# Optimization experiments

Hardware: AMD Instinct MI355X
Metric: run time of the kernel (lower is better)

The kernel has to match this reference:

```python
import jax, jax.numpy as jnp
import numpy as np

N_LAYER = 4
N_HEAD = 16
N_EMBD = 1024
BLOCK = 1024
VOCAB = 100
TRANS = 16          # obs_dim + action_dim + 2 = 11 + 3 + 2
OBS_DIM = 11
ACT_DIM = 3
B, T = 2, 1024
VTOT = VOCAB * TRANS + 1  # token embedding rows
LN_EPS = 1e-5


def _layernorm(x, w, b):
    mu = jnp.mean(x, axis=-1, keepdims=True)
    var = jnp.var(x, axis=-1, keepdims=True)
    return (x - mu) * jax.lax.rsqrt(var + LN_EPS) * w + b


def _build_mask(t):
    # causal tril with every (joined_dim-1 mod joined_dim) column zeroed
    jd = OBS_DIM + ACT_DIM + 2  # 16
    m = jnp.tril(jnp.ones((t, t), dtype=bool))
    cols = jnp.arange(t)
    m = m & ((cols % jd) != (jd - 1))[None, :]
    return m  # [T, T] bool, True = keep


def setup_inputs() -> dict:
    key = jax.random.key(0)
    ks = jax.random.split(key, 24)
    C, L, F4 = N_EMBD, N_LAYER, 4 * N_EMBD
    g = lambda k, s: jax.random.normal(k, s, dtype=jnp.float32) * 0.02
    return {
        "tokens": jax.random.randint(ks[0], (B, T), 0, VTOT),
        "tok_emb": g(ks[1], (VTOT, C)),
        "pos_emb": g(ks[2], (1, BLOCK, C)),
        "Wq": g(ks[3], (L, C, C)), "bq": jnp.zeros((L, C), jnp.float32),
        "Wk": g(ks[4], (L, C, C)), "bk": jnp.zeros((L, C), jnp.float32),
        "Wv": g(ks[5], (L, C, C)), "bv": jnp.zeros((L, C), jnp.float32),
        "Wp": g(ks[6], (L, C, C)), "bp": jnp.zeros((L, C), jnp.float32),
        "ln1w": jnp.ones((L, C), jnp.float32), "ln1b": jnp.zeros((L, C), jnp.float32),
        "ln2w": jnp.ones((L, C), jnp.float32), "ln2b": jnp.zeros((L, C), jnp.float32),
        "W1": g(ks[7], (L, C, F4)), "b1": jnp.zeros((L, F4), jnp.float32),
        "W2": g(ks[8], (L, F4, C)), "b2": jnp.zeros((L, C), jnp.float32),
        "lnfw": jnp.ones((C,), jnp.float32), "lnfb": jnp.zeros((C,), jnp.float32),
        "head_w": g(ks[9], (TRANS, VOCAB + 1, C)),
    }


def _forward(tokens, tok_emb, pos_emb, Wq, bq, Wk, bk, Wv, bv, Wp, bp,
             ln1w, ln1b, ln2w, ln2b, W1, b1, W2, b2, lnfw, lnfb, head_w):
    b, t = tokens.shape
    C, H = N_EMBD, N_HEAD
    D = C // H
    scale = 1.0 / np.sqrt(D)
    mask = _build_mask(t)[None, None]  # [1,1,T,T]

    x = tok_emb[tokens] + pos_emb[:, :t, :]  # [B,T,C]
    for i in range(N_LAYER):
        h = _layernorm(x, ln1w[i], ln1b[i])
        q = (h @ Wq[i] + bq[i]).reshape(b, t, H, D).transpose(0, 2, 1, 3)
        k = (h @ Wk[i] + bk[i]).reshape(b, t, H, D).transpose(0, 2, 1, 3)
        v = (h @ Wv[i] + bv[i]).reshape(b, t, H, D).transpose(0, 2, 1, 3)
        att = jnp.einsum('bhtd,bhsd->bhts', q, k) * scale  # attn_bias=None => +0
        att = jnp.where(mask, att, -jnp.inf)
        att = jax.nn.softmax(att, axis=-1)
        y = jnp.einsum('bhts,bhsd->bhtd', att, v)
        y = y.transpose(0, 2, 1, 3).reshape(b, t, C)
        x = x + (y @ Wp[i] + bp[i])
        h2 = _layernorm(x, ln2w[i], ln2b[i])
        x = x + (jax.nn.gelu(h2 @ W1[i] + b1[i], approximate=False) @ W2[i] + b2[i])

    x = _layernorm(x, lnfw, lnfb)
    # pad_to_full_observation + EinLinear head
    n_pad = (TRANS - t % TRANS) % TRANS
    if n_pad:
        x = jnp.concatenate([x, jnp.zeros((b, n_pad, C), x.dtype)], axis=1)
    x_pad = x.reshape(-1, TRANS, C)                    # [b*n_states, TRANS, C]
    logits = jnp.einsum('eoi,bei->beo', head_w, x_pad)  # EinLinear, bias=False
    logits = logits.reshape(b, t + n_pad, VOCAB + 1)[:, :t]
    return logits


def reference(tokens, tok_emb, pos_emb, Wq, bq, Wk, bk, Wv, bv, Wp, bp,
              ln1w, ln1b, ln2w, ln2b, W1, b1, W2, b2, lnfw, lnfb, head_w):
    return _forward(tokens, tok_emb, pos_emb, Wq, bq, Wk, bk, Wv, bv, Wp, bp,
                    ln1w, ln1b, ln2w, ln2b, W1, b1, W2, b2, lnfw, lnfb, head_w)
```

## Files before the change

### kernel.cpp

```cpp
#include <hip/hip_runtime.h>
#include <hip/hip_bf16.h>
#include <math.h>

typedef unsigned short u16;
typedef __attribute__((ext_vector_type(8))) short short8;
typedef __attribute__((ext_vector_type(4))) short short4v;
typedef __attribute__((ext_vector_type(4))) float f32x4;

#define CDIM 1024
#define TDIM 1024
#define NROWS 2048
#define HEADS 16
#define HD 64
#define F4 4096

__device__ __forceinline__ u16 f2bf(float f) {
    union { float f; unsigned u; } v; v.f = f;
    unsigned r = v.u + 0x7fffu + ((v.u >> 16) & 1u);
    return (u16)(r >> 16);
}
__device__ __forceinline__ float bf2f(u16 h) {
    union { unsigned u; float f; } v; v.u = (unsigned)h << 16; return v.f;
}

__device__ __forceinline__ void gload_lds16(const void* g, void* lds) {
    __builtin_amdgcn_global_load_lds(
        (const __attribute__((address_space(1))) unsigned int*)g,
        (__attribute__((address_space(3))) unsigned int*)lds,
        16, 0, 0);
}

__device__ __forceinline__ void tile_map(int& bx, int& by, int& bz)
{
    const int gx = gridDim.x, gy = gridDim.y;
    const int fid = blockIdx.x + gx * (blockIdx.y + gy * blockIdx.z);
    const int nwg = gx * gy * gridDim.z;
    const int q = nwg >> 3, r = nwg & 7;
    const int xcd = fid & 7, t = fid >> 3;
    const int n = ((xcd < r) ? xcd * (q + 1) : r * (q + 1) + (xcd - r) * q) + t;
    const int nxy = gx * gy;
    bz = n / nxy;
    const int xy = n - bz * nxy;
    const int per_group = gx << 3;
    const int grp = xy / per_group;
    const int in = xy - grp * per_group;
    const int y0 = grp << 3;
    const int rem = gy - y0;
    const int gh = rem < 8 ? rem : 8;
    by = y0 + (in % gh);
    bx = in / gh;
}

__global__ __launch_bounds__(256)
void embed_k(const int* __restrict__ tok, const float* __restrict__ te,
             const float* __restrict__ pe, float* __restrict__ X)
{
    const int row = blockIdx.x;
    const int t = row & (TDIM - 1);
    const int tk = tok[row];
    const int c = threadIdx.x * 4;
    float4 a = *reinterpret_cast<const float4*>(te + (size_t)tk * CDIM + c);
    float4 b = *reinterpret_cast<const float4*>(pe + (size_t)t * CDIM + c);
    a.x += b.x; a.y += b.y; a.z += b.z; a.w += b.w;
    *reinterpret_cast<float4*>(X + (size_t)row * CDIM + c) = a;
}

template<bool BF16OUT>
__global__ __launch_bounds__(256)
void ln_k(const float* __restrict__ X, const float* __restrict__ g,
          const float* __restrict__ be, void* __restrict__ outp)
{
    __shared__ float red[4], red2[4];
    const int row = blockIdx.x, tid = threadIdx.x;
    const float* xr = X + (size_t)row * CDIM;
    const int c = tid * 4;
    float4 xv = *reinterpret_cast<const float4*>(xr + c);
    float s  = xv.x + xv.y + xv.z + xv.w;
    float s2 = xv.x*xv.x + xv.y*xv.y + xv.z*xv.z + xv.w*xv.w;
    #pragma unroll
    for (int off = 32; off; off >>= 1) {
        s  += __shfl_xor(s, off);
        s2 += __shfl_xor(s2, off);
    }
    if ((tid & 63) == 0) { red[tid >> 6] = s; red2[tid >> 6] = s2; }
    __syncthreads();
    const float ts  = red[0] + red[1] + red[2] + red[3];
    const float ts2 = red2[0] + red2[1] + red2[2] + red2[3];
    const float mu  = ts * (1.0f / CDIM);
    const float var = ts2 * (1.0f / CDIM) - mu * mu;
    const float rs  = rsqrtf(var + 1e-5f);
    float4 gv = *reinterpret_cast<const float4*>(g + c);
    float4 bv = *reinterpret_cast<const float4*>(be + c);
    float o0 = (xv.x - mu) * rs * gv.x + bv.x;
    float o1 = (xv.y - mu) * rs * gv.y + bv.y;
    float o2 = (xv.z - mu) * rs * gv.z + bv.z;
    float o3 = (xv.w - mu) * rs * gv.w + bv.w;
    if (BF16OUT) {
        u16 tmp[4] = { f2bf(o0), f2bf(o1), f2bf(o2), f2bf(o3) };
        u16* o = (u16*)outp + (size_t)row * CDIM + c;
        *reinterpret_cast<uint2*>(o) = *reinterpret_cast<const uint2*>(tmp);
    } else {
        float4 ov = { o0, o1, o2, o3 };
        *reinterpret_cast<float4*>((float*)outp + (size_t)row * CDIM + c) = ov;
    }
}

template<int MODE, int NZ>
__global__ __launch_bounds__(256)
void ln_red_k(float* __restrict__ X, const float* __restrict__ P,
              const float* __restrict__ g, const float* __restrict__ be,
              void* __restrict__ outp)
{
    __shared__ float red[4], red2[4];
    const int row = blockIdx.x, tid = threadIdx.x;
    const int c = tid * 4;
    float4 xv = *reinterpret_cast<const float4*>(X + (size_t)row * CDIM + c);
    #pragma unroll
    for (int z = 0; z < NZ; ++z) {
        float4 pv = *reinterpret_cast<const float4*>(P + ((size_t)z * NROWS + row) * CDIM + c);
        xv.x += pv.x; xv.y += pv.y; xv.z += pv.z; xv.w += pv.w;
    }
    if (MODE != 2)
        *reinterpret_cast<float4*>(X + (size_t)row * CDIM + c) = xv;
    float s  = xv.x + xv.y + xv.z + xv.w;
    float s2 = xv.x*xv.x + xv.y*xv.y + xv.z*xv.z + xv.w*xv.w;
    #pragma unroll
    for (int off = 32; off; off >>= 1) {
        s  += __shfl_xor(s, off);
        s2 += __shfl_xor(s2, off);
    }
    if ((tid & 63) == 0) { red[tid >> 6] = s; red2[tid >> 6] = s2; }
    __syncthreads();
    const float ts  = red[0] + red[1] + red[2] + red[3];
    const float ts2 = red2[0] + red2[1] + red2[2] + red2[3];
    const float mu  = ts * (1.0f / CDIM);
    const float var = ts2 * (1.0f / CDIM) - mu * mu;
    const float rs  = rsqrtf(var + 1e-5f);
    float4 gv = *reinterpret_cast<const float4*>(g + c);
    float4 bv = *reinterpret_cast<const float4*>(be + c);
    float o0 = (xv.x - mu) * rs * gv.x + bv.x;
    float o1 = (xv.y - mu) * rs * gv.y + bv.y;
    float o2 = (xv.z - mu) * rs * gv.z + bv.z;
    float o3 = (xv.w - mu) * rs * gv.w + bv.w;
    if (MODE == 0) {
        u16 tmp[4] = { f2bf(o0), f2bf(o1), f2bf(o2), f2bf(o3) };
        u16* o = (u16*)outp + (size_t)row * CDIM + c;
        *reinterpret_cast<uint2*>(o) = *reinterpret_cast<const uint2*>(tmp);
    } else {
        u16 hi[4] = { f2bf(o0), f2bf(o1), f2bf(o2), f2bf(o3) };
        u16 lo[4] = { f2bf(o0 - bf2f(hi[0])), f2bf(o1 - bf2f(hi[1])),
                      f2bf(o2 - bf2f(hi[2])), f2bf(o3 - bf2f(hi[3])) };
        const int b = row >> 10, p = row & 1023;
        const int e = p & 15, slot = p >> 4;
        u16* ar = (u16*)outp + (size_t)(e * 128 + b * 64 + slot) * 3072;
        *reinterpret_cast<uint2*>(ar + c)        = *reinterpret_cast<const uint2*>(hi);
        *reinterpret_cast<uint2*>(ar + 1024 + c) = *reinterpret_cast<const uint2*>(lo);
        *reinterpret_cast<uint2*>(ar + 2048 + c) = *reinterpret_cast<const uint2*>(hi);
    }
}

__global__ __launch_bounds__(256)
void convT_k(const float* __restrict__ W, u16* __restrict__ Wt,
             const int K, const int N)
{
    __shared__ u16 s[64][72];
    const int k0 = blockIdx.y * 64, n0 = blockIdx.x * 64;
    const int tr = threadIdx.x >> 4, tc = (threadIdx.x & 15) * 4;
    #pragma unroll
    for (int i = 0; i < 4; ++i) {
        int r = tr + i * 16;
        float4 w = *reinterpret_cast<const float4*>(W + (size_t)(k0 + r) * N + n0 + tc);
        s[r][tc + 0] = f2bf(w.x); s[r][tc + 1] = f2bf(w.y);
        s[r][tc + 2] = f2bf(w.z); s[r][tc + 3] = f2bf(w.w);
    }
    __syncthreads();
    #pragma unroll
    for (int i = 0; i < 4; ++i) {
        int n = tr + i * 16;
        u16 tmp[4];
        #pragma unroll
        for (int e = 0; e < 4; ++e) tmp[e] = s[tc + e][n];
        *reinterpret_cast<uint2*>(Wt + (size_t)(n0 + n) * K + k0 + tc) =
            *reinterpret_cast<const uint2*>(tmp);
    }
}

__global__ __launch_bounds__(256)
void convT3_k(const float* __restrict__ W0, const float* __restrict__ W1p,
              const float* __restrict__ W2p, u16* __restrict__ Wt)
{
    __shared__ u16 s[64][72];
    const float* W = blockIdx.z == 0 ? W0 : blockIdx.z == 1 ? W1p : W2p;
    u16* dst = Wt + (size_t)blockIdx.z * CDIM * CDIM;
    const int k0 = blockIdx.y * 64, n0 = blockIdx.x * 64;
    const int tr = threadIdx.x >> 4, tc = (threadIdx.x & 15) * 4;
    #pragma unroll
    for (int i = 0; i < 4; ++i) {
        int r = tr + i * 16;
        float4 w = *reinterpret_cast<const float4*>(W + (size_t)(k0 + r) * CDIM + n0 + tc);
        s[r][tc + 0] = f2bf(w.x); s[r][tc + 1] = f2bf(w.y);
        s[r][tc + 2] = f2bf(w.z); s[r][tc + 3] = f2bf(w.w);
    }
    __syncthreads();
    #pragma unroll
    for (int i = 0; i < 4; ++i) {
        int n = tr + i * 16;
        u16 tmp[4];
        #pragma unroll
        for (int e = 0; e < 4; ++e) tmp[e] = s[tc + e][n];
        *reinterpret_cast<uint2*>(dst + (size_t)(n0 + n) * CDIM + k0 + tc) =
            *reinterpret_cast<const uint2*>(tmp);
    }
}

__global__ __launch_bounds__(256)
void conv_head_k(const float* __restrict__ HW, u16* __restrict__ Wt)
{
    const int o = blockIdx.x, e = blockIdx.y;
    const int c = threadIdx.x * 4;
    u16 hi[4] = {0, 0, 0, 0}, lo[4] = {0, 0, 0, 0};
    if (o < 101) {
        float4 w = *reinterpret_cast<const float4*>(HW + ((size_t)e * 101 + o) * 1024 + c);
        hi[0] = f2bf(w.x); hi[1] = f2bf(w.y); hi[2] = f2bf(w.z); hi[3] = f2bf(w.w);
        lo[0] = f2bf(w.x - bf2f(hi[0])); lo[1] = f2bf(w.y - bf2f(hi[1]));
        lo[2] = f2bf(w.z - bf2f(hi[2])); lo[3] = f2bf(w.w - bf2f(hi[3]));
    }
    u16* wr = Wt + (size_t)(e * 128 + o) * 3072;
    *reinterpret_cast<uint2*>(wr + c)        = *reinterpret_cast<const uint2*>(hi);
    *reinterpret_cast<uint2*>(wr + 1024 + c) = *reinterpret_cast<const uint2*>(hi);
    *reinterpret_cast<uint2*>(wr + 2048 + c) = *reinterpret_cast<const uint2*>(lo);
}

__global__ __launch_bounds__(256)
void pack_bias_k(const float* __restrict__ a, const float* __restrict__ b,
                 const float* __restrict__ c, float* __restrict__ o)
{
    const int i = threadIdx.x * 4;
    const float* s = blockIdx.x == 0 ? a : blockIdx.x == 1 ? b : c;
    *reinterpret_cast<float4*>(o + (size_t)blockIdx.x * 1024 + i) =
        *reinterpret_cast<const float4*>(s + i);
}

template<int EPI>
__global__ __launch_bounds__(256, 2)
void gemm_bt(const u16* __restrict__ A, const u16* __restrict__ Bt,
             const float* __restrict__ bias, u16* __restrict__ outb,
             float* __restrict__ resid, u16* __restrict__ vtout,
             const int N, const int K, const int KCH)
{
    __shared__ __align__(16) u16 sA[2][2][128 * 32];
    __shared__ __align__(16) u16 sB[2][2][128 * 32];
    const int tid = threadIdx.x;
    const int lane = tid & 63, wv = tid >> 6;
    int bx, by, bz;
    tile_map(bx, by, bz);
    const int m0 = by * 128, n0 = bx * 128;
    const int kbeg = bz * KCH, kend = bz * KCH + KCH;
    const int fr = lane & 15, fq = lane >> 4;
    const int wm = wv & 1, wn = wv >> 1;
    const int srow = lane >> 2, schunk = (lane & 3) * 8;
    const u16* Bt2 = (EPI == 3) ? Bt + (size_t)by * 128 * K : Bt;
    f32x4 acc[4][4] = {};

    float bias_r[4];
    #pragma unroll
    for (int nj = 0; nj < 4; ++nj) {
        const int col = n0 + wn * 64 + nj * 16 + fr;
        bias_r[nj] = (EPI == 3) ? 0.0f
                     : (EPI == 2 && bz != 0) ? 0.0f : bias[col];
    }

    auto stage = [&](int k0, int buf) {
        #pragma unroll
        for (int kk = 0; kk < 2; ++kk)
            #pragma unroll
            for (int i = 0; i < 2; ++i) {
                const int reg = i * 4 + wv;
                gload_lds16(A  + (size_t)(m0 + reg * 16 + srow) * K + k0 + kk * 32 + schunk,
                            &sA[buf][kk][reg * 512]);
                gload_lds16(Bt2 + (size_t)(n0 + reg * 16 + srow) * K + k0 + kk * 32 + schunk,
                            &sB[buf][kk][reg * 512]);
            }
    };

    asm volatile("s_waitcnt vmcnt(0)" ::: "memory");
    stage(kbeg, 0);
    int cur = 0;
    for (int k0 = kbeg; k0 < kend; k0 += 64) {
        asm volatile("s_waitcnt lgkmcnt(0)" ::: "memory");
        __builtin_amdgcn_s_barrier();
        if (k0 + 64 < kend) {
            stage(k0 + 64, cur ^ 1);
            asm volatile("s_waitcnt vmcnt(8)" ::: "memory");
        } else {
            asm volatile("s_waitcnt vmcnt(0)" ::: "memory");
        }
        __builtin_amdgcn_s_barrier();
        __builtin_amdgcn_s_setprio(1);
        #pragma unroll
        for (int kk = 0; kk < 2; ++kk) {
            short8 af[4], bf[4];
            #pragma unroll
            for (int mi = 0; mi < 4; ++mi)
                af[mi] = *reinterpret_cast<const short8*>(
                    &sA[cur][kk][(wm * 64 + mi * 16 + fr) * 32 + fq * 8]);
            #pragma unroll
            for (int nj = 0; nj < 4; ++nj)
                bf[nj] = *reinterpret_cast<const short8*>(
                    &sB[cur][kk][(wn * 64 + nj * 16 + fr) * 32 + fq * 8]);
            #pragma unroll
            for (int mi = 0; mi < 4; ++mi)
                #pragma unroll
                for (int nj = 0; nj < 4; ++nj)
                    acc[mi][nj] = __builtin_amdgcn_mfma_f32_16x16x32_bf16(af[mi], bf[nj], acc[mi][nj], 0, 0, 0);
        }
        __builtin_amdgcn_s_setprio(0);
        cur ^= 1;
    }

    #pragma unroll
    for (int nj = 0; nj < 4; ++nj) {
        const int col = n0 + wn * 64 + nj * 16 + fr;
        const float bias_v = bias_r[nj];
        #pragma unroll
        for (int mi = 0; mi < 4; ++mi) {
            const int rowb = m0 + wm * 64 + mi * 16 + fq * 4;
            if (EPI == 0 && vtout != nullptr && col >= 2048) {
                const int bidx = rowb >> 10, t = rowb & 1023, hd = col - 2048;
                u16 t4[4];
                #pragma unroll
                for (int r = 0; r < 4; ++r) t4[r] = f2bf(acc[mi][nj][r] + bias_v);
                *reinterpret_cast<uint2*>(
                    vtout + ((size_t)(bidx * 16 + (hd >> 6)) * 64 + (hd & 63)) * 1024 + t) =
                    *reinterpret_cast<const uint2*>(t4);
            } else {
                #pragma unroll
                for (int r = 0; r < 4; ++r) {
                    const int row = rowb + r;
                    float cv = acc[mi][nj][r] + bias_v;
                    if (EPI == 0) {
                        outb[(size_t)row * N + col] = f2bf(cv);
                    } else if (EPI == 1) {
                        float gl = 0.5f * cv * (1.0f + erff(cv * 0.70710678118654752f));
                        outb[(size_t)row * N + col] = f2bf(gl);
                    } else if (EPI == 2) {
                        resid[((size_t)bz * NROWS + row) * N + col] = cv;
                    } else {
                        resid[((size_t)bz * NROWS + row) * 128 + col] = cv;
                    }
                }
            }
        }
    }
}

__global__ __launch_bounds__(128)
void head_red_k(const float* __restrict__ P, float* __restrict__ out)
{
    const int pr = blockIdx.x;
    const int col = threadIdx.x;
    const int e = pr >> 7, rem = pr & 127, b = rem >> 6, slot = rem & 63;
    float s = 0.0f;
    #pragma unroll
    for (int z = 0; z < 8; ++z)
        s += P[((size_t)z * NROWS + pr) * 128 + col];
    if (col < 101)
        out[((size_t)(b << 10) + (slot << 4) + e) * 101 + col] = s;
}

__global__ __launch_bounds__(256, 4)
void attn_k(const u16* __restrict__ QKV, const u16* __restrict__ VT,
            float* __restrict__ po, float* __restrict__ plsum)
{
    __shared__ __align__(16) u16 sK[2][64][72];
    __shared__ __align__(16) u16 sV[2][64][72];
    const int tid = threadIdx.x, lane = tid & 63, wv = tid >> 6;
    const int fr = lane & 15, fq = lane >> 4;
    int bx, by, bz;
    tile_map(bx, by, bz);
    const int qt = bx, h = by, b = bz >> 1, sc = bz & 1;
    const int q0 = qt * 64;
    const int nt = qt + 1, h1 = (nt + 1) >> 1;
    const int stbeg = sc ? h1 : 0, stend = sc ? nt : h1;
    const u16* Qb = QKV + (size_t)b * TDIM * 3072 + h * HD;
    const u16* Vb = VT + ((size_t)(b * HEADS + h) * HD) * TDIM;
    const int r0 = tid >> 3, c0 = (tid & 7) * 8;

    const u16* qp = Qb + (size_t)(q0 + wv * 16 + fr) * 3072 + fq * 8;
    short8 aQ0 = *reinterpret_cast<const short8*>(qp);
    short8 aQ1 = *reinterpret_cast<const short8*>(qp + 32);

    f32x4 o[4] = {};
    float lsum = 0.0f;
    int cur = 0;

    if (stbeg < stend) {
        #pragma unroll
        for (int i = 0; i < 2; ++i) {
            const int r = r0 + i * 32;
            *reinterpret_cast<uint4*>(&sK[0][r][c0]) =
                *reinterpret_cast<const uint4*>(Qb + 1024 + (size_t)(stbeg * 64 + r) * 3072 + c0);
            *reinterpret_cast<uint4*>(&sV[0][r][c0]) =
                *reinterpret_cast<const uint4*>(Vb + (size_t)r * TDIM + stbeg * 64 + c0);
        }
        __syncthreads();
    }

    for (int st = stbeg; st < stend; ++st) {
        const int s0 = st * 64;
        const bool pf = (st + 1) < stend;
        uint4 pk[2], pv[2];
        if (pf) {
            #pragma unroll
            for (int i = 0; i < 2; ++i) {
                const int r = r0 + i * 32;
                pk[i] = *reinterpret_cast<const uint4*>(Qb + 1024 + (size_t)(s0 + 64 + r) * 3072 + c0);
                pv[i] = *reinterpret_cast<const uint4*>(Vb + (size_t)r * TDIM + s0 + 64 + c0);
            }
        }
        f32x4 sacc[4] = {};
        #pragma unroll
        for (int j = 0; j < 4; ++j) {
            short8 k0f = *reinterpret_cast<const short8*>(&sK[cur][j * 16 + fr][fq * 8]);
            sacc[j] = __builtin_amdgcn_mfma_f32_16x16x32_bf16(k0f, aQ0, sacc[j], 0, 0, 0);
            short8 k1f = *reinterpret_cast<const short8*>(&sK[cur][j * 16 + fr][32 + fq * 8]);
            sacc[j] = __builtin_amdgcn_mfma_f32_16x16x32_bf16(k1f, aQ1, sacc[j], 0, 0, 0);
        }
        const int qrow = q0 + wv * 16 + fr;
        u16 pb[4][4];
        #pragma unroll
        for (int j = 0; j < 4; ++j)
            #pragma unroll
            for (int r = 0; r < 4; ++r) {
                const int scol = s0 + j * 16 + fq * 4 + r;
                const bool keep = (scol <= qrow) && ((scol & 15) != 15);
                const float p = keep ? __expf(sacc[j][r] * 0.125f) : 0.0f;
                const u16 hb = f2bf(p);
                pb[j][r] = hb;
                lsum += bf2f(hb);
            }
        union { unsigned u[4]; short8 v; } a0, a1;
        a0.u[0] = (unsigned)pb[0][0] | ((unsigned)pb[0][1] << 16);
        a0.u[1] = (unsigned)pb[0][2] | ((unsigned)pb[0][3] << 16);
        a0.u[2] = (unsigned)pb[1][0] | ((unsigned)pb[1][1] << 16);
        a0.u[3] = (unsigned)pb[1][2] | ((unsigned)pb[1][3] << 16);
        a1.u[0] = (unsigned)pb[2][0] | ((unsigned)pb[2][1] << 16);
        a1.u[1] = (unsigned)pb[2][2] | ((unsigned)pb[2][3] << 16);
        a1.u[2] = (unsigned)pb[3][0] | ((unsigned)pb[3][1] << 16);
        a1.u[3] = (unsigned)pb[3][2] | ((unsigned)pb[3][3] << 16);
        #pragma unroll
        for (int j = 0; j < 4; ++j) {
            const u16* vrow = &sV[cur][j * 16 + fr][0];
            short4v v0 = *reinterpret_cast<const short4v*>(vrow + fq * 4);
            short4v v1 = *reinterpret_cast<const short4v*>(vrow + 16 + fq * 4);
            short8 bV0 = __builtin_shufflevector(v0, v1, 0, 1, 2, 3, 4, 5, 6, 7);
            o[j] = __builtin_amdgcn_mfma_f32_16x16x32_bf16(a0.v, bV0, o[j], 0, 0, 0);
            short4v v2 = *reinterpret_cast<const short4v*>(vrow + 32 + fq * 4);
            short4v v3 = *reinterpret_cast<const short4v*>(vrow + 48 + fq * 4);
            short8 bV1 = __builtin_shufflevector(v2, v3, 0, 1, 2, 3, 4, 5, 6, 7);
            o[j] = __builtin_amdgcn_mfma_f32_16x16x32_bf16(a1.v, bV1, o[j], 0, 0, 0);
        }
        if (pf) {
            #pragma unroll
            for (int i = 0; i < 2; ++i) {
                const int r = r0 + i * 32;
                *reinterpret_cast<uint4*>(&sK[cur ^ 1][r][c0]) = pk[i];
                *reinterpret_cast<uint4*>(&sV[cur ^ 1][r][c0]) = pv[i];
            }
            __syncthreads();
            cur ^= 1;
        }
    }

    lsum += __shfl_xor(lsum, 16);
    lsum += __shfl_xor(lsum, 32);

    const int tl = (bz * 16 + h) * 16 + qt;
    float* pt = po + (size_t)tl * 4096;
    #pragma unroll
    for (int j = 0; j < 4; ++j)
        #pragma unroll
        for (int r = 0; r < 4; ++r)
            pt[(wv * 16 + fq * 4 + r) * 64 + j * 16 + fr] = o[j][r];
    if (fq == 0) plsum[(size_t)tl * 64 + wv * 16 + fr] = lsum;
}

__global__ __launch_bounds__(256)
void attn_comb_k(const float* __restrict__ po, const float* __restrict__ plsum,
                 u16* __restrict__ Y)
{
    const int qt = blockIdx.x, h = blockIdx.y, b = blockIdx.z;
    const int t0 = ((b * 2 + 0) * 16 + h) * 16 + qt;
    const int t1 = ((b * 2 + 1) * 16 + h) * 16 + qt;
    const float* p0 = po + (size_t)t0 * 4096;
    const float* p1 = po + (size_t)t1 * 4096;
    const float* l0 = plsum + (size_t)t0 * 64;
    const float* l1 = plsum + (size_t)t1 * 64;
    #pragma unroll
    for (int i = 0; i < 4; ++i) {
        const int f4 = threadIdx.x + i * 256;
        const int q = f4 >> 4, d4 = (f4 & 15) * 4;
        float4 a = *reinterpret_cast<const float4*>(p0 + f4 * 4);
        float4 c = *reinterpret_cast<const float4*>(p1 + f4 * 4);
        const float rl = 1.0f / (l0[q] + l1[q]);
        u16 t4[4] = { f2bf((a.x + c.x) * rl), f2bf((a.y + c.y) * rl),
                      f2bf((a.z + c.z) * rl), f2bf((a.w + c.w) * rl) };
        *reinterpret_cast<uint2*>(
            Y + ((size_t)(b * TDIM + qt * 64 + q)) * CDIM + h * HD + d4) =
            *reinterpret_cast<const uint2*>(t4);
    }
}

extern "C" void kernel_launch(void* const* d_in, const int* in_sizes, int n_in,
                              void* d_out, int out_size, void* d_ws, size_t ws_size,
                              hipStream_t stream)
{
    const int*   tokens = (const int*)  d_in[0];
    const float* tok_emb= (const float*)d_in[1];
    const float* pos_emb= (const float*)d_in[2];
    const float* Wq = (const float*)d_in[3];
    const float* bq = (const float*)d_in[4];
    const float* Wk = (const float*)d_in[5];
    const float* bk = (const float*)d_in[6];
    const float* Wv = (const float*)d_in[7];
    const float* bv = (const float*)d_in[8];
    const float* Wp = (const float*)d_in[9];
    const float* bp = (const float*)d_in[10];
    const float* ln1w = (const float*)d_in[11];
    const float* ln1b = (const float*)d_in[12];
    const float* ln2w = (const float*)d_in[13];
    const float* ln2b = (const float*)d_in[14];
    const float* W1 = (const float*)d_in[15];
    const float* b1 = (const float*)d_in[16];
    const float* W2 = (const float*)d_in[17];
    const float* b2 = (const float*)d_in[18];
    const float* lnfw = (const float*)d_in[19];
    const float* lnfb = (const float*)d_in[20];
    const float* head_w = (const float*)d_in[21];
    float* out = (float*)d_out;

    char* ws = (char*)d_ws;
    float* x    = (float*)(ws);
    float* hpart= (float*)(ws);
    u16*   hbuf = (u16*)  (ws + (8u  << 20));
    u16*   yb   = (u16*)  (ws + (8u  << 20));
    u16*   qkv  = (u16*)  (ws + (12u << 20));
    u16*   xg   = (u16*)  (ws + (12u << 20));
    u16*   vt   = (u16*)  (ws + (24u << 20));
    u16*   mid  = (u16*)  (ws + (12u << 20));
    u16*   wbuf = (u16*)  (ws + (28u << 20));
    float* pbuf = (float*)(ws + (36u << 20));
    u16*   whp  = (u16*)  (ws + (36u << 20));
    float* po   = (float*)(ws + (36u << 20));
    float* plsum= (float*)(ws + (53u << 20));
    float* bbuf = (float*)(ws + (100u << 20));

    embed_k<<<NROWS, 256, 0, stream>>>(tokens, tok_emb, pos_emb, x);

    for (int l = 0; l < 4; ++l) {
        const size_t wo = (size_t)l * CDIM * CDIM;
        convT3_k<<<dim3(16, 16, 3), 256, 0, stream>>>(Wq + wo, Wk + wo, Wv + wo, wbuf);
        pack_bias_k<<<3, 256, 0, stream>>>(bq + l * CDIM, bk + l * CDIM, bv + l * CDIM, bbuf);

        if (l == 0)
            ln_k<true><<<NROWS, 256, 0, stream>>>(x, ln1w, ln1b, hbuf);
        else
            ln_red_k<0, 4><<<NROWS, 256, 0, stream>>>(x, pbuf, ln1w + l * CDIM, ln1b + l * CDIM, hbuf);
        gemm_bt<0><<<dim3(24, 16, 1), 256, 0, stream>>>(hbuf, wbuf, bbuf, qkv, nullptr, vt, 3072, CDIM, CDIM);
        attn_k<<<dim3(16, HEADS, 4), 256, 0, stream>>>(qkv, vt, po, plsum);
        attn_comb_k<<<dim3(16, HEADS, 2), 256, 0, stream>>>(po, plsum, yb);

        convT_k<<<dim3(16, 16), 256, 0, stream>>>(Wp + wo, wbuf, CDIM, CDIM);
        gemm_bt<2><<<dim3(8, 16, 2), 256, 0, stream>>>(yb, wbuf, bp + l * CDIM, nullptr, pbuf, nullptr, CDIM, CDIM, 512);

        ln_red_k<0, 2><<<NROWS, 256, 0, stream>>>(x, pbuf, ln2w + l * CDIM, ln2b + l * CDIM, hbuf);
        convT_k<<<dim3(64, 16), 256, 0, stream>>>(W1 + (size_t)l * CDIM * F4, wbuf, CDIM, F4);
        gemm_bt<1><<<dim3(32, 16, 1), 256, 0, stream>>>(hbuf, wbuf, b1 + l * F4, mid, nullptr, nullptr, F4, CDIM, CDIM);
        convT_k<<<dim3(16, 64), 256, 0, stream>>>(W2 + (size_t)l * F4 * CDIM, wbuf, F4, CDIM);
        gemm_bt<2><<<dim3(8, 16, 4), 256, 0, stream>>>(mid, wbuf, b2 + l * CDIM, nullptr, pbuf, nullptr, CDIM, F4, CDIM);
    }

    ln_red_k<2, 4><<<NROWS, 256, 0, stream>>>(x, pbuf, lnfw, lnfb, xg);
    conv_head_k<<<dim3(128, 16), 256, 0, stream>>>(head_w, whp);
    gemm_bt<3><<<dim3(1, 16, 8), 256, 0, stream>>>(xg, whp, nullptr, nullptr, hpart, nullptr, 128, 3072, 384);
    head_red_k<<<NROWS, 128, 0, stream>>>(hpart, out);
}
```

Measured before the change: 932.4 us.

## Swizzle GEMM LDS chunks and split attention KV range four ways

The GEMM's LDS staging now XOR-swizzles the 16-byte chunk index by row bits, and the fragment reads use the matching swizzle. This is meant to avoid LDS bank conflicts on the MFMA operand loads. Separately, attention now splits each query tile's key range into four chunks instead of two, giving more blocks for the causal workload. The combine kernel now merges four partials, and the partial-sum buffer moves to make room. The extra split adds partial traffic and empty blocks for early query tiles.

```diff
diff --git a/kernel.cpp b/kernel.cpp
--- a/kernel.cpp
+++ b/kernel.cpp
@@ -258,7 +258,9 @@
     const int kbeg = bz * KCH, kend = bz * KCH + KCH;
     const int fr = lane & 15, fq = lane >> 4;
     const int wm = wv & 1, wn = wv >> 1;
-    const int srow = lane >> 2, schunk = (lane & 3) * 8;
+    const int srow = lane >> 2;
+    const int schunk = (((lane & 3) ^ ((lane >> 3) & 3)) * 8);
+    const int csw = (fr >> 1) & 3;
     const u16* Bt2 = (EPI == 3) ? Bt + (size_t)by * 128 * K : Bt;
     f32x4 acc[4][4] = {};
 
@@ -303,11 +305,11 @@
             #pragma unroll
             for (int mi = 0; mi < 4; ++mi)
                 af[mi] = *reinterpret_cast<const short8*>(
-                    &sA[cur][kk][(wm * 64 + mi * 16 + fr) * 32 + fq * 8]);
+                    &sA[cur][kk][(wm * 64 + mi * 16 + fr) * 32 + (fq ^ csw) * 8]);
             #pragma unroll
             for (int nj = 0; nj < 4; ++nj)
                 bf[nj] = *reinterpret_cast<const short8*>(
-                    &sB[cur][kk][(wn * 64 + nj * 16 + fr) * 32 + fq * 8]);
+                    &sB[cur][kk][(wn * 64 + nj * 16 + fr) * 32 + (fq ^ csw) * 8]);
             #pragma unroll
             for (int mi = 0; mi < 4; ++mi)
                 #pragma unroll
@@ -378,10 +380,10 @@
     const int fr = lane & 15, fq = lane >> 4;
     int bx, by, bz;
     tile_map(bx, by, bz);
-    const int qt = bx, h = by, b = bz >> 1, sc = bz & 1;
+    const int qt = bx, h = by, b = bz >> 2, sc = bz & 3;
     const int q0 = qt * 64;
-    const int nt = qt + 1, h1 = (nt + 1) >> 1;
-    const int stbeg = sc ? h1 : 0, stend = sc ? nt : h1;
+    const int nt = qt + 1;
+    const int stbeg = (nt * sc) >> 2, stend = (nt * (sc + 1)) >> 2;
     const u16* Qb = QKV + (size_t)b * TDIM * 3072 + h * HD;
     const u16* Vb = VT + ((size_t)(b * HEADS + h) * HD) * TDIM;
     const int r0 = tid >> 3, c0 = (tid & 7) * 8;
@@ -490,21 +492,24 @@
                  u16* __restrict__ Y)
 {
     const int qt = blockIdx.x, h = blockIdx.y, b = blockIdx.z;
-    const int t0 = ((b * 2 + 0) * 16 + h) * 16 + qt;
-    const int t1 = ((b * 2 + 1) * 16 + h) * 16 + qt;
-    const float* p0 = po + (size_t)t0 * 4096;
-    const float* p1 = po + (size_t)t1 * 4096;
-    const float* l0 = plsum + (size_t)t0 * 64;
-    const float* l1 = plsum + (size_t)t1 * 64;
+    int t[4];
+    #pragma unroll
+    for (int i = 0; i < 4; ++i) t[i] = ((b * 4 + i) * 16 + h) * 16 + qt;
     #pragma unroll
     for (int i = 0; i < 4; ++i) {
         const int f4 = threadIdx.x + i * 256;
         const int q = f4 >> 4, d4 = (f4 & 15) * 4;
-        float4 a = *reinterpret_cast<const float4*>(p0 + f4 * 4);
-        float4 c = *reinterpret_cast<const float4*>(p1 + f4 * 4);
-        const float rl = 1.0f / (l0[q] + l1[q]);
-        u16 t4[4] = { f2bf((a.x + c.x) * rl), f2bf((a.y + c.y) * rl),
-                      f2bf((a.z + c.z) * rl), f2bf((a.w + c.w) * rl) };
+        float4 a = *reinterpret_cast<const float4*>(po + (size_t)t[0] * 4096 + f4 * 4);
+        float ls = plsum[(size_t)t[0] * 64 + q];
+        #pragma unroll
+        for (int k = 1; k < 4; ++k) {
+            float4 c = *reinterpret_cast<const float4*>(po + (size_t)t[k] * 4096 + f4 * 4);
+            a.x += c.x; a.y += c.y; a.z += c.z; a.w += c.w;
+            ls += plsum[(size_t)t[k] * 64 + q];
+        }
+        const float rl = 1.0f / ls;
+        u16 t4[4] = { f2bf(a.x * rl), f2bf(a.y * rl),
+                      f2bf(a.z * rl), f2bf(a.w * rl) };
         *reinterpret_cast<uint2*>(
             Y + ((size_t)(b * TDIM + qt * 64 + q)) * CDIM + h * HD + d4) =
             *reinterpret_cast<const uint2*>(t4);
@@ -552,7 +557,7 @@
     float* pbuf = (float*)(ws + (36u << 20));
     u16*   whp  = (u16*)  (ws + (36u << 20));
     float* po   = (float*)(ws + (36u << 20));
-    float* plsum= (float*)(ws + (53u << 20));
+    float* plsum= (float*)(ws + (68u << 20));
     float* bbuf = (float*)(ws + (100u << 20));
 
     embed_k<<<NROWS, 256, 0, stream>>>(tokens, tok_emb, pos_emb, x);
@@ -567,7 +572,7 @@
         else
             ln_red_k<0, 4><<<NROWS, 256, 0, stream>>>(x, pbuf, ln1w + l * CDIM, ln1b + l * CDIM, hbuf);
         gemm_bt<0><<<dim3(24, 16, 1), 256, 0, stream>>>(hbuf, wbuf, bbuf, qkv, nullptr, vt, 3072, CDIM, CDIM);
-        attn_k<<<dim3(16, HEADS, 4), 256, 0, stream>>>(qkv, vt, po, plsum);
+        attn_k<<<dim3(16, HEADS, 8), 256, 0, stream>>>(qkv, vt, po, plsum);
         attn_comb_k<<<dim3(16, HEADS, 2), 256, 0, stream>>>(po, plsum, yb);
 
         convT_k<<<dim3(16, 16), 256, 0, stream>>>(Wp + wo, wbuf, CDIM, CDIM);
```

After: 918.6 us. No clear change (-1.5%).
